# Performance work log

Hardware: AMD Instinct MI355X
Metric: run time of the kernel (lower is better)

Reference implementation:

```python
import jax, jax.numpy as jnp
import numpy as np

B, N, DIM, H, DH, K = 4, 2048, 512, 6, 64, 16
KEEP_PROB = 0.9  # 1 - dropout_rate
LOG2PI = float(np.log(2.0 * np.pi))
LOG_PRIOR = float(np.log(1.0 / K))


def setup_inputs() -> dict:
    key = jax.random.key(0)
    ks = jax.random.split(key, 7)
    inputs_q = jax.random.normal(ks[0], (B, N, DIM), dtype=jnp.float32)
    # decoder-style causal mask, shape [B, 1, q_len, kv_len]
    causal = jnp.tril(jnp.ones((N, N), dtype=jnp.float32))
    mask = jnp.broadcast_to(causal[None, None], (B, 1, N, N))
    # dropout keep mask broadcast across the query dim: [B, H, 1, kv_len]
    keep = jax.random.bernoulli(ks[1], KEEP_PROB, (B, H, 1, N)).astype(jnp.float32)
    w_qkv = jax.random.normal(ks[2], (DIM, 3 * H * DH), dtype=jnp.float32) * 0.02
    w_out = jax.random.normal(ks[3], (H * DH, DIM), dtype=jnp.float32) * 0.02
    mu_lookup = jax.random.normal(ks[4], (K, DIM), dtype=jnp.float32)
    logvar_lookup = jax.random.normal(ks[5], (K, DIM), dtype=jnp.float32) * 0.1
    return {
        "inputs_q": inputs_q,
        "mask": mask,
        "keep": keep,
        "w_qkv": w_qkv,
        "w_out": w_out,
        "mu_lookup": mu_lookup,
        "logvar_lookup": logvar_lookup,
    }


def reference(inputs_q, mask, keep, w_qkv, w_out, mu_lookup, logvar_lookup):
    # --- MultiHeadDotProductAttention (self-attn path) ---
    qkv = (inputs_q @ w_qkv).reshape(B, N, 3, H, DH)  # [B,N,3,H,DH]
    q, k, v = qkv[:, :, 0], qkv[:, :, 1], qkv[:, :, 2]
    # bias: 0 where mask > 0, -1e10 elsewhere (note: no 1/sqrt(d) scaling, as in source)
    bias = jnp.where(mask > 0, 0.0, -1e10)
    attn_weights = jnp.einsum('bqhd,bkhd->bhqk', q, k) + bias  # [B,H,N,N]
    attn_weights = jax.nn.softmax(attn_weights, axis=-1)
    # broadcast dropout: mask shared across the query dim
    attn_weights = attn_weights * keep / KEEP_PROB
    attn_out = jnp.einsum('bhqk,bkhd->bqhd', attn_weights, v)
    attn_out = attn_out.reshape(B, N, H * DH) @ w_out  # [B,N,DIM]

    # --- GMM posterior approx q(y|x) ~= p(y|z) (approx_qy_x, vectorized over k) ---
    z = attn_out.mean(axis=1)  # pooled latent, [B,DIM]
    diff = z[:, None, :] - mu_lookup[None]  # [B,K,DIM]
    llh = -0.5 * jnp.sum(
        diff * diff / jnp.exp(logvar_lookup)[None] + logvar_lookup[None] + LOG2PI,
        axis=-1,
    )  # [B,K]
    logLogit_qy_x = llh + LOG_PRIOR
    qy_x = jax.nn.softmax(logLogit_qy_x, axis=1)  # [B,K]

    # combine mixture mean back in so both branches are live in one output
    return attn_out + (qy_x @ mu_lookup)[:, None, :]
```

## Files before the change

### kernel.cpp

```cpp
#include <hip/hip_runtime.h>
#include <cstdint>
#include <cstddef>

#define NH 6
#define NSEQ 2048
#define DIMD 512
#define BATCH 4
#define HD 384
#define LOG2PI_F 1.8378770664093453f

typedef __attribute__((ext_vector_type(8))) short short8;
typedef __attribute__((ext_vector_type(8))) unsigned short ushort8;
typedef __attribute__((ext_vector_type(4))) unsigned short ushort4v;
typedef __attribute__((ext_vector_type(4))) float floatx4;

__device__ inline unsigned short f2bf(float f){
  unsigned int u = __float_as_uint(f);
  u += 0x7FFFu + ((u>>16)&1u);
  return (unsigned short)(u>>16);
}

#define GLD16(gp, lp) __builtin_amdgcn_global_load_lds( \
  (const __attribute__((address_space(1))) void*)(gp), \
  (__attribute__((address_space(3))) void*)(lp), 16, 0, 0)

__global__ __launch_bounds__(256) void convert_x(
    const float* __restrict__ xq, unsigned short* __restrict__ xbf)
{
  int i = blockIdx.x*256 + threadIdx.x;
  floatx4 v = *(const floatx4*)(xq + (size_t)i*4);
  ushort4v r;
  #pragma unroll
  for(int j=0;j<4;j++) r[j] = f2bf(v[j]);
  *(ushort4v*)(xbf + (size_t)i*4) = r;
}

__global__ __launch_bounds__(256) void wtrans(
    const float* __restrict__ src, unsigned short* __restrict__ dst, int R, int C)
{
  __shared__ __attribute__((aligned(16))) unsigned short Ls[64*72];
  const int t = threadIdx.x;
  const int r = t>>2, c0 = (t&3)*16;
  const int d0 = blockIdx.y*64, n0 = blockIdx.x*64;
  #pragma unroll
  for (int j=0;j<16;j+=4){
    floatx4 v = *(const floatx4*)(src + (size_t)(d0+r)*C + n0 + c0 + j);
    #pragma unroll
    for(int jj=0;jj<4;jj++) Ls[r*72 + c0+j+jj] = f2bf(v[jj]);
  }
  __syncthreads();
  #pragma unroll
  for (int j=0;j<16;j+=8){
    ushort8 o;
    #pragma unroll
    for(int jj=0;jj<8;jj++) o[jj] = Ls[(c0+j+jj)*72 + r];
    *(ushort8*)(dst + (size_t)(n0+r)*R + d0 + c0 + j) = o;
  }
}

__global__ __launch_bounds__(256) void vtrans(
    const unsigned short* __restrict__ Vo, unsigned short* __restrict__ Vt)
{
  __shared__ __attribute__((aligned(16))) unsigned short Ls[64*72];
  const int t = threadIdx.x;
  const int r = t>>2, c0 = (t&3)*16;
  const int n0 = blockIdx.x*64, bh = blockIdx.y;
  #pragma unroll
  for (int j=0;j<16;j+=8)
    *(ushort8*)(Ls + r*72 + c0 + j) = *(const ushort8*)(Vo + ((size_t)bh*NSEQ + n0 + r)*64 + c0 + j);
  __syncthreads();
  #pragma unroll
  for (int j=0;j<16;j+=8){
    ushort8 o;
    #pragma unroll
    for(int jj=0;jj<8;jj++) o[jj] = Ls[(c0+j+jj)*72 + r];
    *(ushort8*)(Vt + ((size_t)bh*64 + r)*NSEQ + n0 + c0 + j) = o;
  }
}

__global__ __launch_bounds__(256) void gemm_qkv(
    const unsigned short* __restrict__ A,
    const unsigned short* __restrict__ Bt,
    const float* __restrict__ keep,
    unsigned short* __restrict__ Qo, unsigned short* __restrict__ Ko, unsigned short* __restrict__ Vo)
{
  __shared__ __attribute__((aligned(16))) unsigned short Cs[128*132];
  unsigned short* As = Cs;
  unsigned short* Bs = Cs + 128*64;
  const int tid = threadIdx.x;
  const int w = tid>>6, lane = tid&63;
  const int wr = w>>1, wc = w&1;
  const int quad = lane>>4, l16 = lane&15;
  const int tM = blockIdx.x*128, tN = blockIdx.y*128;
  const int r8 = lane>>3, c8 = (lane&7)*8;
  floatx4 acc[4][4];
  floatx4 zed = {0.f,0.f,0.f,0.f};
  #pragma unroll
  for (int i=0;i<4;i++)
    #pragma unroll
    for(int j=0;j<4;j++) acc[i][j] = zed;

  for (int k0=0; k0<512; k0+=64){
    #pragma unroll
    for (int i=0;i<4;i++){
      int row = w*32 + i*8;
      GLD16(A  + (size_t)(tM+row+r8)*512 + k0 + c8, As + row*64);
      GLD16(Bt + (size_t)(tN+row+r8)*512 + k0 + c8, Bs + row*64);
    }
    __syncthreads();
    #pragma unroll
    for (int kk=0; kk<64; kk+=32){
      short8 af[4], bf[4];
      #pragma unroll
      for(int mt=0;mt<4;mt++)
        af[mt] = *(const short8*)(As + (wr*64+mt*16+l16)*64 + kk + quad*8);
      #pragma unroll
      for(int nt=0;nt<4;nt++)
        bf[nt] = *(const short8*)(Bs + (wc*64+nt*16+l16)*64 + kk + quad*8);
      #pragma unroll
      for(int mt=0;mt<4;mt++)
        #pragma unroll
        for(int nt=0;nt<4;nt++)
          acc[mt][nt] = __builtin_amdgcn_mfma_f32_16x16x32_bf16(af[mt], bf[nt], acc[mt][nt], 0,0,0);
    }
    __syncthreads();
  }
  #pragma unroll
  for(int mt=0;mt<4;mt++)
    #pragma unroll
    for(int nt=0;nt<4;nt++)
      #pragma unroll
      for(int r=0;r<4;r++)
        Cs[(wr*64+mt*16+quad*4+r)*132 + wc*64+nt*16+l16] = f2bf(acc[mt][nt][r]);
  __syncthreads();
  const int row = tid>>1, colh = (tid&1)*64;
  const int gcol0 = tN + colh;
  const int t = gcol0/384, rem = gcol0 - t*384, h = rem>>6;
  const int grow = tM + row, b = grow>>11, n = grow & 2047;
  unsigned short* dst = (t==0 ? Qo : (t==1 ? Ko : Vo)) + ((size_t)((b*NH+h)*NSEQ+n))*64;
  bool vzero = false;
  if (t==2) vzero = (keep[(size_t)(b*NH+h)*NSEQ+n] < 0.5f);
  ushort8 zz;
  #pragma unroll
  for(int q2=0;q2<8;q2++) zz[q2]=0;
  #pragma unroll
  for(int j=0;j<8;j++){
    ushort8 v = *(const ushort8*)(Cs + row*132 + colh + j*8);
    *(ushort8*)(dst + j*8) = vzero ? zz : v;
  }
}

__global__ __launch_bounds__(64) void attn_kernel(
    const unsigned short* __restrict__ Qg, const unsigned short* __restrict__ Kg,
    const unsigned short* __restrict__ VtG,
    unsigned short* __restrict__ atp)
{
  __shared__ __attribute__((aligned(16))) unsigned short Ps[32*72];
  const int lane = threadIdx.x;
  const int quad = lane>>4, l16 = lane&15;
  const int bid = blockIdx.x;
  const int idx = bid>>3;
  const int bh  = (bid&7) + 8*(idx % 3);
  const int c   = 63 - idx/3;
  const int b = bh/NH, h = bh - b*NH;
  const unsigned short* Qb = Qg  + (size_t)bh*NSEQ*64;
  const unsigned short* Kb = Kg  + (size_t)bh*NSEQ*64;
  const unsigned short* Vb = VtG + (size_t)bh*64*NSEQ;
  const int q0 = c*32;
  const int nkt = (c>>1) + 1;

  short8 qf[2][2];
  #pragma unroll
  for(int mt=0;mt<2;mt++)
    #pragma unroll
    for(int kc=0;kc<2;kc++)
      qf[mt][kc] = *(const short8*)(Qb + (size_t)(q0+mt*16+l16)*64 + kc*32 + quad*8);

  short8 onesf;
  #pragma unroll
  for(int j=0;j<8;j++) onesf[j] = (short)0x3F80;

  floatx4 O[2][4];
  floatx4 accl[2];
  floatx4 zed = {0.f,0.f,0.f,0.f};
  #pragma unroll
  for(int mt=0;mt<2;mt++){
    #pragma unroll
    for(int dt=0;dt<4;dt++) O[mt][dt] = zed;
    accl[mt] = zed;
  }

  short8 kA[4][2], kB2[4][2];
  auto loadK = [&](int kt, short8 (&kf)[4][2]){
    const unsigned short* kp0 = Kb + (size_t)kt*64*64;
    #pragma unroll
    for(int nt=0;nt<4;nt++)
      #pragma unroll
      for(int kc=0;kc<2;kc++)
        kf[nt][kc] = *(const short8*)(kp0 + (size_t)(nt*16+l16)*64 + kc*32 + quad*8);
  };

  auto tile = [&](int kt, short8 (&kf)[4][2]){
    const int kB = kt*64;
    short8 vf[2][4];
    const unsigned short* vp0 = Vb + kB;
    #pragma unroll
    for(int kh=0;kh<2;kh++)
      #pragma unroll
      for(int dt=0;dt<4;dt++)
        vf[kh][dt] = *(const short8*)(vp0 + (size_t)(dt*16+l16)*NSEQ + kh*32 + quad*8);

    floatx4 sacc[2][4];
    floatx4 m12 = {-12.f,-12.f,-12.f,-12.f};
    #pragma unroll
    for(int mt=0;mt<2;mt++)
      #pragma unroll
      for(int nt=0;nt<4;nt++) sacc[mt][nt] = m12;
    #pragma unroll
    for(int mt=0;mt<2;mt++)
      #pragma unroll
      for(int nt=0;nt<4;nt++)
        #pragma unroll
        for(int kc=0;kc<2;kc++)
          sacc[mt][nt] = __builtin_amdgcn_mfma_f32_16x16x32_bf16(qf[mt][kc], kf[nt][kc], sacc[mt][nt], 0,0,0);

    const bool dia = (kt == nkt-1);
    #pragma unroll
    for(int mt=0;mt<2;mt++){
      #pragma unroll
      for(int nt=0;nt<4;nt++){
        int key = kB + nt*16 + l16;
        #pragma unroll
        for(int r=0;r<4;r++){
          float p = __expf(sacc[mt][nt][r]);
          if (dia) p = (key <= q0 + mt*16 + quad*4 + r) ? p : 0.f;
          Ps[(mt*16+quad*4+r)*72 + nt*16 + l16] = f2bf(p);
        }
      }
    }
    #pragma unroll
    for(int kh=0;kh<2;kh++){
      #pragma unroll
      for(int mt=0;mt<2;mt++){
        short8 pf = *(const short8*)(Ps + (mt*16+l16)*72 + kh*32 + quad*8);
        accl[mt] = __builtin_amdgcn_mfma_f32_16x16x32_bf16(pf, onesf, accl[mt], 0,0,0);
        #pragma unroll
        for(int dt=0;dt<4;dt++)
          O[mt][dt] = __builtin_amdgcn_mfma_f32_16x16x32_bf16(pf, vf[kh][dt], O[mt][dt], 0,0,0);
      }
    }
  };

  loadK(0, kA);
  int kt = 0;
  while (true){
    loadK(kt+1 < nkt ? kt+1 : kt, kB2);
    tile(kt, kA);
    kt++; if (kt >= nkt) break;
    loadK(kt+1 < nkt ? kt+1 : kt, kA);
    tile(kt, kB2);
    kt++; if (kt >= nkt) break;
  }

  #pragma unroll
  for(int mt=0;mt<2;mt++)
    #pragma unroll
    for(int r=0;r<4;r++){
      float sc2 = (1.0f/0.9f) / accl[mt][r];
      #pragma unroll
      for(int dt=0;dt<4;dt++)
        Ps[(mt*16+quad*4+r)*72 + dt*16 + l16] = f2bf(O[mt][dt][r]*sc2);
    }
  const int orow = lane>>1, ohalf = (lane&1)*32;
  const int q = q0 + orow;
  unsigned short* dstp = atp + ((size_t)(b*NSEQ+q))*HD + h*64 + ohalf;
  #pragma unroll
  for(int j=0;j<4;j++)
    *(ushort8*)(dstp + j*8) = *(const ushort8*)(Ps + orow*72 + ohalf + j*8);
}

__global__ __launch_bounds__(256) void gemm_proj(
    const unsigned short* __restrict__ A,
    const unsigned short* __restrict__ Bt,
    float* __restrict__ out,
    float* __restrict__ z)
{
  __shared__ __attribute__((aligned(16))) unsigned short As[128*64];
  __shared__ __attribute__((aligned(16))) unsigned short Bs[128*64];
  const int tid = threadIdx.x;
  const int w = tid>>6, lane = tid&63;
  const int wr = w>>1, wc = w&1;
  const int quad = lane>>4, l16 = lane&15;
  const int tM = blockIdx.x*128, tN = blockIdx.y*128;
  const int r8 = lane>>3, c8 = (lane&7)*8;
  floatx4 acc[4][4];
  floatx4 zed = {0.f,0.f,0.f,0.f};
  #pragma unroll
  for (int i=0;i<4;i++)
    #pragma unroll
    for(int j=0;j<4;j++) acc[i][j] = zed;

  for (int k0=0; k0<384; k0+=64){
    #pragma unroll
    for (int i=0;i<4;i++){
      int row = w*32 + i*8;
      GLD16(A  + (size_t)(tM+row+r8)*384 + k0 + c8, As + row*64);
      GLD16(Bt + (size_t)(tN+row+r8)*384 + k0 + c8, Bs + row*64);
    }
    __syncthreads();
    #pragma unroll
    for (int kk=0; kk<64; kk+=32){
      short8 af[4], bf[4];
      #pragma unroll
      for(int mt=0;mt<4;mt++)
        af[mt] = *(const short8*)(As + (wr*64+mt*16+l16)*64 + kk + quad*8);
      #pragma unroll
      for(int nt=0;nt<4;nt++)
        bf[nt] = *(const short8*)(Bs + (wc*64+nt*16+l16)*64 + kk + quad*8);
      #pragma unroll
      for(int mt=0;mt<4;mt++)
        #pragma unroll
        for(int nt=0;nt<4;nt++)
          acc[mt][nt] = __builtin_amdgcn_mfma_f32_16x16x32_bf16(af[mt], bf[nt], acc[mt][nt], 0,0,0);
    }
    __syncthreads();
  }
  #pragma unroll
  for(int mt=0;mt<4;mt++){
    int grow = tM + wr*64 + mt*16 + quad*4;
    #pragma unroll
    for(int nt=0;nt<4;nt++){
      int gcol = tN + wc*64 + nt*16 + l16;
      #pragma unroll
      for(int r=0;r<4;r++)
        out[(size_t)(grow+r)*512 + gcol] = acc[mt][nt][r];
    }
  }
  #pragma unroll
  for(int nt=0;nt<4;nt++){
    float s = 0.f;
    #pragma unroll
    for(int mt=0;mt<4;mt++)
      #pragma unroll
      for(int r=0;r<4;r++) s += acc[mt][nt][r];
    s += __shfl_xor(s, 16, 64);
    s += __shfl_xor(s, 32, 64);
    if (quad == 0){
      int gcol = tN + wc*64 + nt*16 + l16;
      atomicAdd(&z[(tM>>11)*DIMD + gcol], s);
    }
  }
}

__global__ __launch_bounds__(256) void gmm_kernel(
    const float* __restrict__ z, const float* __restrict__ mu,
    const float* __restrict__ lv, float* __restrict__ c)
{
  __shared__ float sh[16];
  __shared__ float qy[16];
  int tid = threadIdx.x;
  int k = tid>>4, li = tid&15;
  int b = blockIdx.x;
  float part = 0.f;
  for(int d=li; d<DIMD; d+=16){
    float zz = z[b*DIMD+d] * (1.0f/2048.0f);
    float m = mu[k*DIMD+d], l = lv[k*DIMD+d];
    float diff = zz - m;
    part += diff*diff*__expf(-l) + l + LOG2PI_F;
  }
  #pragma unroll
  for(int off=8;off>=1;off>>=1) part += __shfl_xor(part, off, 64);
  if (li==0) sh[k] = part;
  __syncthreads();
  if (tid<16){
    float logit = -0.5f*sh[tid];
    float mx = logit;
    #pragma unroll
    for(int off=8;off>=1;off>>=1) mx = fmaxf(mx, __shfl_xor(mx, off, 64));
    float e = __expf(logit-mx);
    float se = e;
    #pragma unroll
    for(int off=8;off>=1;off>>=1) se += __shfl_xor(se, off, 64);
    qy[tid] = e/se;
  }
  __syncthreads();
  for(int d=tid; d<DIMD; d+=256){
    float accv = 0.f;
    #pragma unroll
    for(int kk=0;kk<16;kk++) accv += qy[kk]*mu[kk*DIMD+d];
    c[b*DIMD+d] = accv;
  }
}

__global__ __launch_bounds__(256) void final_add(
    float* __restrict__ out, const float* __restrict__ c)
{
  size_t i = ((size_t)blockIdx.x*256 + threadIdx.x)*4;
  int d = (int)(i & 511);
  int b = (int)(i >> 20);
  floatx4 a = *(const floatx4*)(out + i);
  floatx4 cc = *(const floatx4*)(c + b*DIMD + d);
  *(floatx4*)(out + i) = a + cc;
}

extern "C" void kernel_launch(void* const* d_in, const int* in_sizes, int n_in,
                              void* d_out, int out_size, void* d_ws, size_t ws_size,
                              hipStream_t stream) {
  const float* inputs_q = (const float*)d_in[0];
  const float* keep  = (const float*)d_in[2];
  const float* w_qkv = (const float*)d_in[3];
  const float* w_out = (const float*)d_in[4];
  const float* mu    = (const float*)d_in[5];
  const float* lv    = (const float*)d_in[6];
  float* out = (float*)d_out;
  char* ws = (char*)d_ws;
  size_t off = 0;
  auto alloc = [&](size_t bytes){ void* p = ws + off; off += (bytes + 255) & ~(size_t)255; return p; };
  unsigned short* Qb  = (unsigned short*)alloc((size_t)24*2048*64*2);
  unsigned short* Kb  = (unsigned short*)alloc((size_t)24*2048*64*2);
  unsigned short* Vo  = (unsigned short*)alloc((size_t)24*2048*64*2);
  unsigned short* Vt  = (unsigned short*)alloc((size_t)24*64*2048*2);
  unsigned short* xbf = (unsigned short*)alloc((size_t)8192*512*2);
  unsigned short* wqT = (unsigned short*)alloc((size_t)1152*512*2);
  unsigned short* woT = (unsigned short*)alloc((size_t)512*384*2);
  unsigned short* atp = (unsigned short*)alloc((size_t)8192*384*2);
  float* z  = (float*)alloc((size_t)4*512*4);
  float* c  = (float*)alloc((size_t)4*512*4);

  hipMemsetAsync(z, 0, 4*512*4, stream);
  convert_x<<<4096, 256, 0, stream>>>(inputs_q, xbf);
  wtrans<<<dim3(18,8), 256, 0, stream>>>(w_qkv, wqT, 512, 1152);
  wtrans<<<dim3(8,6),  256, 0, stream>>>(w_out, woT, 384, 512);
  gemm_qkv<<<dim3(64,9), 256, 0, stream>>>(xbf, wqT, keep, Qb, Kb, Vo);
  vtrans<<<dim3(32,24), 256, 0, stream>>>(Vo, Vt);
  attn_kernel<<<1536, 64, 0, stream>>>(Qb, Kb, Vt, atp);
  gemm_proj<<<dim3(64,4), 256, 0, stream>>>(atp, woT, out, z);
  gmm_kernel<<<4, 256, 0, stream>>>(z, mu, lv, c);
  final_add<<<4096, 256, 0, stream>>>(out, c);
}
```

Baseline: 246.3 us.

## Fuse prep kernels, write V transposed from QKV GEMM, pool z in attention

The conversion, weight-transpose and zeroing kernels are merged into one launch. The QKV GEMM now writes V already transposed and dropout-scaled, so the separate vtrans pass and its Vo buffer go away. Attention is cut to 16-query tiles, doubling the number of blocks. Each attention block atomically accumulates its pooled head output into zA, and the GMM kernel computes z by multiplying zA with w_out instead of reading projection outputs. The mixture mean is added in the projection epilogue, which removes the final_add pass over the output. The trade-offs are more atomics, a serial 384-long dot product per column in the GMM kernel, a truncating bf16 conversion of P, and GMM now sitting on the critical path before the projection GEMM.

```diff
diff --git a/kernel.cpp b/kernel.cpp
--- a/kernel.cpp
+++ b/kernel.cpp
@@ -13,6 +13,7 @@
 typedef __attribute__((ext_vector_type(8))) unsigned short ushort8;
 typedef __attribute__((ext_vector_type(4))) unsigned short ushort4v;
 typedef __attribute__((ext_vector_type(4))) float floatx4;
+typedef __attribute__((ext_vector_type(2))) unsigned int uint2v;
 
 __device__ inline unsigned short f2bf(float f){
   unsigned int u = __float_as_uint(f);
@@ -24,57 +25,46 @@
   (const __attribute__((address_space(1))) void*)(gp), \
   (__attribute__((address_space(3))) void*)(lp), 16, 0, 0)
 
-__global__ __launch_bounds__(256) void convert_x(
-    const float* __restrict__ xq, unsigned short* __restrict__ xbf)
-{
-  int i = blockIdx.x*256 + threadIdx.x;
-  floatx4 v = *(const floatx4*)(xq + (size_t)i*4);
-  ushort4v r;
-  #pragma unroll
-  for(int j=0;j<4;j++) r[j] = f2bf(v[j]);
-  *(ushort4v*)(xbf + (size_t)i*4) = r;
-}
-
-__global__ __launch_bounds__(256) void wtrans(
-    const float* __restrict__ src, unsigned short* __restrict__ dst, int R, int C)
+__global__ __launch_bounds__(256) void prep_kernel(
+    const float* __restrict__ xq, const float* __restrict__ wq, const float* __restrict__ wo,
+    unsigned short* __restrict__ xbf, unsigned short* __restrict__ wqT,
+    unsigned short* __restrict__ woT, float* __restrict__ zA)
 {
   __shared__ __attribute__((aligned(16))) unsigned short Ls[64*72];
-  const int t = threadIdx.x;
-  const int r = t>>2, c0 = (t&3)*16;
-  const int d0 = blockIdx.y*64, n0 = blockIdx.x*64;
-  #pragma unroll
-  for (int j=0;j<16;j+=4){
-    floatx4 v = *(const floatx4*)(src + (size_t)(d0+r)*C + n0 + c0 + j);
-    #pragma unroll
-    for(int jj=0;jj<4;jj++) Ls[r*72 + c0+j+jj] = f2bf(v[jj]);
-  }
-  __syncthreads();
-  #pragma unroll
-  for (int j=0;j<16;j+=8){
-    ushort8 o;
-    #pragma unroll
-    for(int jj=0;jj<8;jj++) o[jj] = Ls[(c0+j+jj)*72 + r];
-    *(ushort8*)(dst + (size_t)(n0+r)*R + d0 + c0 + j) = o;
-  }
-}
-
-__global__ __launch_bounds__(256) void vtrans(
-    const unsigned short* __restrict__ Vo, unsigned short* __restrict__ Vt)
-{
-  __shared__ __attribute__((aligned(16))) unsigned short Ls[64*72];
-  const int t = threadIdx.x;
-  const int r = t>>2, c0 = (t&3)*16;
-  const int n0 = blockIdx.x*64, bh = blockIdx.y;
-  #pragma unroll
-  for (int j=0;j<16;j+=8)
-    *(ushort8*)(Ls + r*72 + c0 + j) = *(const ushort8*)(Vo + ((size_t)bh*NSEQ + n0 + r)*64 + c0 + j);
-  __syncthreads();
-  #pragma unroll
-  for (int j=0;j<16;j+=8){
-    ushort8 o;
-    #pragma unroll
-    for(int jj=0;jj<8;jj++) o[jj] = Ls[(c0+j+jj)*72 + r];
-    *(ushort8*)(Vt + ((size_t)bh*64 + r)*NSEQ + n0 + c0 + j) = o;
+  const int bid = blockIdx.x, t = threadIdx.x;
+  if (bid < 4096){
+    int i = bid*256 + t;
+    floatx4 v = *(const floatx4*)(xq + (size_t)i*4);
+    ushort4v r;
+    #pragma unroll
+    for(int j=0;j<4;j++) r[j] = f2bf(v[j]);
+    *(ushort4v*)(xbf + (size_t)i*4) = r;
+  } else if (bid < 4096+144+48){
+    const bool isq = bid < 4096+144;
+    const int j  = isq ? bid-4096 : bid-(4096+144);
+    const int nx = isq ? 18 : 8;
+    const int R  = isq ? 512 : 384, C = isq ? 1152 : 512;
+    const float* src = isq ? wq : wo;
+    unsigned short* dst = isq ? wqT : woT;
+    const int x = j % nx, y = j / nx;
+    const int n0 = x*64, d0 = y*64;
+    const int r = t>>2, c0 = (t&3)*16;
+    #pragma unroll
+    for (int jj=0;jj<16;jj+=4){
+      floatx4 v = *(const floatx4*)(src + (size_t)(d0+r)*C + n0 + c0 + jj);
+      #pragma unroll
+      for(int q=0;q<4;q++) Ls[r*72 + c0+jj+q] = f2bf(v[q]);
+    }
+    __syncthreads();
+    #pragma unroll
+    for (int jj=0;jj<16;jj+=8){
+      ushort8 o;
+      #pragma unroll
+      for(int q=0;q<8;q++) o[q] = Ls[(c0+jj+q)*72 + r];
+      *(ushort8*)(dst + (size_t)(n0+r)*R + d0 + c0 + jj) = o;
+    }
+  } else {
+    for (int i=t; i<BATCH*HD; i+=256) zA[i] = 0.f;
   }
 }
 
@@ -82,16 +72,17 @@
     const unsigned short* __restrict__ A,
     const unsigned short* __restrict__ Bt,
     const float* __restrict__ keep,
-    unsigned short* __restrict__ Qo, unsigned short* __restrict__ Ko, unsigned short* __restrict__ Vo)
+    unsigned short* __restrict__ Qo, unsigned short* __restrict__ Ko, unsigned short* __restrict__ Vt)
 {
-  __shared__ __attribute__((aligned(16))) unsigned short Cs[128*132];
+  __shared__ __attribute__((aligned(16))) unsigned short Cs[128*136];
   unsigned short* As = Cs;
   unsigned short* Bs = Cs + 128*64;
   const int tid = threadIdx.x;
   const int w = tid>>6, lane = tid&63;
   const int wr = w>>1, wc = w&1;
   const int quad = lane>>4, l16 = lane&15;
-  const int tM = blockIdx.x*128, tN = blockIdx.y*128;
+  const int by = blockIdx.y;
+  const int tM = blockIdx.x*128, tN = by*128;
   const int r8 = lane>>3, c8 = (lane&7)*8;
   floatx4 acc[4][4];
   floatx4 zed = {0.f,0.f,0.f,0.f};
@@ -125,70 +116,89 @@
     }
     __syncthreads();
   }
-  #pragma unroll
-  for(int mt=0;mt<4;mt++)
-    #pragma unroll
-    for(int nt=0;nt<4;nt++)
-      #pragma unroll
-      for(int r=0;r<4;r++)
-        Cs[(wr*64+mt*16+quad*4+r)*132 + wc*64+nt*16+l16] = f2bf(acc[mt][nt][r]);
-  __syncthreads();
-  const int row = tid>>1, colh = (tid&1)*64;
-  const int gcol0 = tN + colh;
-  const int t = gcol0/384, rem = gcol0 - t*384, h = rem>>6;
-  const int grow = tM + row, b = grow>>11, n = grow & 2047;
-  unsigned short* dst = (t==0 ? Qo : (t==1 ? Ko : Vo)) + ((size_t)((b*NH+h)*NSEQ+n))*64;
-  bool vzero = false;
-  if (t==2) vzero = (keep[(size_t)(b*NH+h)*NSEQ+n] < 0.5f);
-  ushort8 zz;
-  #pragma unroll
-  for(int q2=0;q2<8;q2++) zz[q2]=0;
-  #pragma unroll
-  for(int j=0;j<8;j++){
-    ushort8 v = *(const ushort8*)(Cs + row*132 + colh + j*8);
-    *(ushort8*)(dst + j*8) = vzero ? zz : v;
+  const int b = tM>>11;
+  if (by < 6){
+    #pragma unroll
+    for(int mt=0;mt<4;mt++)
+      #pragma unroll
+      for(int nt=0;nt<4;nt++)
+        #pragma unroll
+        for(int r=0;r<4;r++)
+          Cs[(wr*64+mt*16+quad*4+r)*132 + wc*64+nt*16+l16] = f2bf(acc[mt][nt][r]);
+    __syncthreads();
+    const int row = tid>>1, colh = (tid&1)*64;
+    const int gcol0 = tN + colh;
+    const int tq = gcol0/384, rem = gcol0 - tq*384, h = rem>>6;
+    const int grow = tM + row, n = grow & 2047;
+    unsigned short* dst = (tq==0 ? Qo : Ko) + ((size_t)((b*NH+h)*NSEQ+n))*64;
+    #pragma unroll
+    for(int j=0;j<8;j++)
+      *(ushort8*)(dst + j*8) = *(const ushort8*)(Cs + row*132 + colh + j*8);
+  } else {
+    const int hbase = (by-6)*2;
+    const float* kp = keep + (size_t)(b*NH + hbase + wc)*NSEQ + (tM & 2047);
+    #pragma unroll
+    for(int mt=0;mt<4;mt++){
+      float kv[4];
+      #pragma unroll
+      for(int r=0;r<4;r++) kv[r] = kp[wr*64+mt*16+quad*4+r];
+      #pragma unroll
+      for(int nt=0;nt<4;nt++){
+        int col = wc*64+nt*16+l16;
+        int row = wr*64+mt*16+quad*4;
+        unsigned int lo = (unsigned int)f2bf(acc[mt][nt][0]*kv[0]) | ((unsigned int)f2bf(acc[mt][nt][1]*kv[1])<<16);
+        unsigned int hi = (unsigned int)f2bf(acc[mt][nt][2]*kv[2]) | ((unsigned int)f2bf(acc[mt][nt][3]*kv[3])<<16);
+        uint2v v2 = {lo, hi};
+        *(uint2v*)(Cs + (size_t)col*136 + row) = v2;
+      }
+    }
+    __syncthreads();
+    const int nu = tid & 15;
+    #pragma unroll
+    for(int vc0=0; vc0<128; vc0+=16){
+      int vtcol = vc0 + (tid>>4);
+      int h2 = hbase + (vtcol>>6), dh = vtcol & 63;
+      unsigned short* dstv = Vt + ((size_t)((b*NH+h2)*64 + dh))*NSEQ + (tM & 2047) + nu*8;
+      *(ushort8*)dstv = *(const ushort8*)(Cs + (size_t)vtcol*136 + nu*8);
+    }
   }
 }
 
 __global__ __launch_bounds__(64) void attn_kernel(
     const unsigned short* __restrict__ Qg, const unsigned short* __restrict__ Kg,
     const unsigned short* __restrict__ VtG,
-    unsigned short* __restrict__ atp)
+    unsigned short* __restrict__ atp,
+    float* __restrict__ zA)
 {
-  __shared__ __attribute__((aligned(16))) unsigned short Ps[32*72];
+  __shared__ __attribute__((aligned(16))) unsigned short Ps[16*72];
   const int lane = threadIdx.x;
   const int quad = lane>>4, l16 = lane&15;
   const int bid = blockIdx.x;
   const int idx = bid>>3;
   const int bh  = (bid&7) + 8*(idx % 3);
-  const int c   = 63 - idx/3;
+  const int c   = 127 - idx/3;
   const int b = bh/NH, h = bh - b*NH;
   const unsigned short* Qb = Qg  + (size_t)bh*NSEQ*64;
   const unsigned short* Kb = Kg  + (size_t)bh*NSEQ*64;
   const unsigned short* Vb = VtG + (size_t)bh*64*NSEQ;
-  const int q0 = c*32;
-  const int nkt = (c>>1) + 1;
-
-  short8 qf[2][2];
-  #pragma unroll
-  for(int mt=0;mt<2;mt++)
-    #pragma unroll
-    for(int kc=0;kc<2;kc++)
-      qf[mt][kc] = *(const short8*)(Qb + (size_t)(q0+mt*16+l16)*64 + kc*32 + quad*8);
+  const int q0 = c*16;
+  const int nkt = (c>>2) + 1;
+
+  short8 qf[2];
+  #pragma unroll
+  for(int kc=0;kc<2;kc++)
+    qf[kc] = *(const short8*)(Qb + (size_t)(q0+l16)*64 + kc*32 + quad*8);
 
   short8 onesf;
   #pragma unroll
   for(int j=0;j<8;j++) onesf[j] = (short)0x3F80;
 
-  floatx4 O[2][4];
-  floatx4 accl[2];
+  floatx4 O[4];
+  floatx4 accl;
   floatx4 zed = {0.f,0.f,0.f,0.f};
   #pragma unroll
-  for(int mt=0;mt<2;mt++){
-    #pragma unroll
-    for(int dt=0;dt<4;dt++) O[mt][dt] = zed;
-    accl[mt] = zed;
-  }
+  for(int dt=0;dt<4;dt++) O[dt] = zed;
+  accl = zed;
 
   short8 kA[4][2], kB2[4][2];
   auto loadK = [&](int kt, short8 (&kf)[4][2]){
@@ -210,44 +220,34 @@
       for(int dt=0;dt<4;dt++)
         vf[kh][dt] = *(const short8*)(vp0 + (size_t)(dt*16+l16)*NSEQ + kh*32 + quad*8);
 
-    floatx4 sacc[2][4];
+    floatx4 sacc[4];
     floatx4 m12 = {-12.f,-12.f,-12.f,-12.f};
     #pragma unroll
-    for(int mt=0;mt<2;mt++)
-      #pragma unroll
-      for(int nt=0;nt<4;nt++) sacc[mt][nt] = m12;
-    #pragma unroll
-    for(int mt=0;mt<2;mt++)
-      #pragma unroll
-      for(int nt=0;nt<4;nt++)
-        #pragma unroll
-        for(int kc=0;kc<2;kc++)
-          sacc[mt][nt] = __builtin_amdgcn_mfma_f32_16x16x32_bf16(qf[mt][kc], kf[nt][kc], sacc[mt][nt], 0,0,0);
+    for(int nt=0;nt<4;nt++) sacc[nt] = m12;
+    #pragma unroll
+    for(int nt=0;nt<4;nt++)
+      #pragma unroll
+      for(int kc=0;kc<2;kc++)
+        sacc[nt] = __builtin_amdgcn_mfma_f32_16x16x32_bf16(qf[kc], kf[nt][kc], sacc[nt], 0,0,0);
 
     const bool dia = (kt == nkt-1);
     #pragma unroll
-    for(int mt=0;mt<2;mt++){
-      #pragma unroll
-      for(int nt=0;nt<4;nt++){
-        int key = kB + nt*16 + l16;
-        #pragma unroll
-        for(int r=0;r<4;r++){
-          float p = __expf(sacc[mt][nt][r]);
-          if (dia) p = (key <= q0 + mt*16 + quad*4 + r) ? p : 0.f;
-          Ps[(mt*16+quad*4+r)*72 + nt*16 + l16] = f2bf(p);
-        }
+    for(int nt=0;nt<4;nt++){
+      int key = kB + nt*16 + l16;
+      #pragma unroll
+      for(int r=0;r<4;r++){
+        float p = __expf(sacc[nt][r]);
+        if (dia) p = (key <= q0 + quad*4 + r) ? p : 0.f;
+        Ps[(quad*4+r)*72 + nt*16 + l16] = (unsigned short)(__float_as_uint(p)>>16);
       }
     }
     #pragma unroll
     for(int kh=0;kh<2;kh++){
-      #pragma unroll
-      for(int mt=0;mt<2;mt++){
-        short8 pf = *(const short8*)(Ps + (mt*16+l16)*72 + kh*32 + quad*8);
-        accl[mt] = __builtin_amdgcn_mfma_f32_16x16x32_bf16(pf, onesf, accl[mt], 0,0,0);
-        #pragma unroll
-        for(int dt=0;dt<4;dt++)
-          O[mt][dt] = __builtin_amdgcn_mfma_f32_16x16x32_bf16(pf, vf[kh][dt], O[mt][dt], 0,0,0);
-      }
+      short8 pf = *(const short8*)(Ps + l16*72 + kh*32 + quad*8);
+      accl = __builtin_amdgcn_mfma_f32_16x16x32_bf16(pf, onesf, accl, 0,0,0);
+      #pragma unroll
+      for(int dt=0;dt<4;dt++)
+        O[dt] = __builtin_amdgcn_mfma_f32_16x16x32_bf16(pf, vf[kh][dt], O[dt], 0,0,0);
     }
   };
 
@@ -262,28 +262,80 @@
     kt++; if (kt >= nkt) break;
   }
 
-  #pragma unroll
-  for(int mt=0;mt<2;mt++)
+  float sc2[4];
+  #pragma unroll
+  for(int r=0;r<4;r++) sc2[r] = (1.0f/0.9f) / accl[r];
+  #pragma unroll
+  for(int dt=0;dt<4;dt++){
+    float s = 0.f;
     #pragma unroll
     for(int r=0;r<4;r++){
-      float sc2 = (1.0f/0.9f) / accl[mt][r];
-      #pragma unroll
-      for(int dt=0;dt<4;dt++)
-        Ps[(mt*16+quad*4+r)*72 + dt*16 + l16] = f2bf(O[mt][dt][r]*sc2);
-    }
-  const int orow = lane>>1, ohalf = (lane&1)*32;
-  const int q = q0 + orow;
-  unsigned short* dstp = atp + ((size_t)(b*NSEQ+q))*HD + h*64 + ohalf;
-  #pragma unroll
-  for(int j=0;j<4;j++)
-    *(ushort8*)(dstp + j*8) = *(const ushort8*)(Ps + orow*72 + ohalf + j*8);
+      float v = O[dt][r]*sc2[r];
+      s += v;
+      Ps[(quad*4+r)*72 + dt*16 + l16] = f2bf(v);
+    }
+    atomicAdd(&zA[b*HD + h*64 + dt*16 + l16], s);
+  }
+  const int orow = lane>>2, oseg = (lane&3)*16;
+  unsigned short* dstp = atp + ((size_t)(b*NSEQ + q0 + orow))*HD + h*64 + oseg;
+  *(ushort8*)(dstp)     = *(const ushort8*)(Ps + orow*72 + oseg);
+  *(ushort8*)(dstp + 8) = *(const ushort8*)(Ps + orow*72 + oseg + 8);
+}
+
+__global__ __launch_bounds__(256) void gmm_kernel(
+    const float* __restrict__ zA, const float* __restrict__ wo,
+    const float* __restrict__ mu, const float* __restrict__ lv, float* __restrict__ c)
+{
+  __shared__ float zAs[HD];
+  __shared__ float zs[DIMD];
+  __shared__ float sh[16];
+  __shared__ float qy[16];
+  const int tid = threadIdx.x;
+  const int b = blockIdx.x;
+  for (int i=tid; i<HD; i+=256) zAs[i] = zA[b*HD + i];
+  __syncthreads();
+  for (int d=tid; d<DIMD; d+=256){
+    float s = 0.f;
+    for (int k=0; k<HD; k++) s += zAs[k]*wo[(size_t)k*DIMD + d];
+    zs[d] = s * (1.0f/2048.0f);
+  }
+  __syncthreads();
+  const int k = tid>>4, li = tid&15;
+  float part = 0.f;
+  for(int d=li; d<DIMD; d+=16){
+    float m = mu[k*DIMD+d], l = lv[k*DIMD+d];
+    float diff = zs[d] - m;
+    part += diff*diff*__expf(-l) + l + LOG2PI_F;
+  }
+  #pragma unroll
+  for(int off=8;off>=1;off>>=1) part += __shfl_xor(part, off, 64);
+  if (li==0) sh[k] = part;
+  __syncthreads();
+  if (tid<16){
+    float logit = -0.5f*sh[tid];
+    float mx = logit;
+    #pragma unroll
+    for(int off=8;off>=1;off>>=1) mx = fmaxf(mx, __shfl_xor(mx, off, 64));
+    float e = __expf(logit-mx);
+    float se = e;
+    #pragma unroll
+    for(int off=8;off>=1;off>>=1) se += __shfl_xor(se, off, 64);
+    qy[tid] = e/se;
+  }
+  __syncthreads();
+  for(int d=tid; d<DIMD; d+=256){
+    float accv = 0.f;
+    #pragma unroll
+    for(int kk=0;kk<16;kk++) accv += qy[kk]*mu[kk*DIMD+d];
+    c[b*DIMD+d] = accv;
+  }
 }
 
 __global__ __launch_bounds__(256) void gemm_proj(
     const unsigned short* __restrict__ A,
     const unsigned short* __restrict__ Bt,
-    float* __restrict__ out,
-    float* __restrict__ z)
+    const float* __restrict__ c,
+    float* __restrict__ out)
 {
   __shared__ __attribute__((aligned(16))) unsigned short As[128*64];
   __shared__ __attribute__((aligned(16))) unsigned short Bs[128*64];
@@ -325,6 +377,10 @@
     }
     __syncthreads();
   }
+  const int b = tM>>11;
+  float cb[4];
+  #pragma unroll
+  for(int nt=0;nt<4;nt++) cb[nt] = c[b*DIMD + tN + wc*64 + nt*16 + l16];
   #pragma unroll
   for(int mt=0;mt<4;mt++){
     int grow = tM + wr*64 + mt*16 + quad*4;
@@ -333,74 +389,9 @@
       int gcol = tN + wc*64 + nt*16 + l16;
       #pragma unroll
       for(int r=0;r<4;r++)
-        out[(size_t)(grow+r)*512 + gcol] = acc[mt][nt][r];
-    }
-  }
-  #pragma unroll
-  for(int nt=0;nt<4;nt++){
-    float s = 0.f;
-    #pragma unroll
-    for(int mt=0;mt<4;mt++)
-      #pragma unroll
-      for(int r=0;r<4;r++) s += acc[mt][nt][r];
-    s += __shfl_xor(s, 16, 64);
-    s += __shfl_xor(s, 32, 64);
-    if (quad == 0){
-      int gcol = tN + wc*64 + nt*16 + l16;
-      atomicAdd(&z[(tM>>11)*DIMD + gcol], s);
-    }
-  }
-}
-
-__global__ __launch_bounds__(256) void gmm_kernel(
-    const float* __restrict__ z, const float* __restrict__ mu,
-    const float* __restrict__ lv, float* __restrict__ c)
-{
-  __shared__ float sh[16];
-  __shared__ float qy[16];
-  int tid = threadIdx.x;
-  int k = tid>>4, li = tid&15;
-  int b = blockIdx.x;
-  float part = 0.f;
-  for(int d=li; d<DIMD; d+=16){
-    float zz = z[b*DIMD+d] * (1.0f/2048.0f);
-    float m = mu[k*DIMD+d], l = lv[k*DIMD+d];
-    float diff = zz - m;
-    part += diff*diff*__expf(-l) + l + LOG2PI_F;
-  }
-  #pragma unroll
-  for(int off=8;off>=1;off>>=1) part += __shfl_xor(part, off, 64);
-  if (li==0) sh[k] = part;
-  __syncthreads();
-  if (tid<16){
-    float logit = -0.5f*sh[tid];
-    float mx = logit;
-    #pragma unroll
-    for(int off=8;off>=1;off>>=1) mx = fmaxf(mx, __shfl_xor(mx, off, 64));
-    float e = __expf(logit-mx);
-    float se = e;
-    #pragma unroll
-    for(int off=8;off>=1;off>>=1) se += __shfl_xor(se, off, 64);
-    qy[tid] = e/se;
-  }
-  __syncthreads();
-  for(int d=tid; d<DIMD; d+=256){
-    float accv = 0.f;
-    #pragma unroll
-    for(int kk=0;kk<16;kk++) accv += qy[kk]*mu[kk*DIMD+d];
-    c[b*DIMD+d] = accv;
-  }
-}
-
-__global__ __launch_bounds__(256) void final_add(
-    float* __restrict__ out, const float* __restrict__ c)
-{
-  size_t i = ((size_t)blockIdx.x*256 + threadIdx.x)*4;
-  int d = (int)(i & 511);
-  int b = (int)(i >> 20);
-  floatx4 a = *(const floatx4*)(out + i);
-  floatx4 cc = *(const floatx4*)(c + b*DIMD + d);
-  *(floatx4*)(out + i) = a + cc;
+        out[(size_t)(grow+r)*512 + gcol] = acc[mt][nt][r] + cb[nt];
+    }
+  }
 }
 
 extern "C" void kernel_launch(void* const* d_in, const int* in_sizes, int n_in,
@@ -418,23 +409,17 @@
   auto alloc = [&](size_t bytes){ void* p = ws + off; off += (bytes + 255) & ~(size_t)255; return p; };
   unsigned short* Qb  = (unsigned short*)alloc((size_t)24*2048*64*2);
   unsigned short* Kb  = (unsigned short*)alloc((size_t)24*2048*64*2);
-  unsigned short* Vo  = (unsigned short*)alloc((size_t)24*2048*64*2);
   unsigned short* Vt  = (unsigned short*)alloc((size_t)24*64*2048*2);
   unsigned short* xbf = (unsigned short*)alloc((size_t)8192*512*2);
   unsigned short* wqT = (unsigned short*)alloc((size_t)1152*512*2);
   unsigned short* woT = (unsigned short*)alloc((size_t)512*384*2);
   unsigned short* atp = (unsigned short*)alloc((size_t)8192*384*2);
-  float* z  = (float*)alloc((size_t)4*512*4);
+  float* zA = (float*)alloc((size_t)4*384*4);
   float* c  = (float*)alloc((size_t)4*512*4);
 
-  hipMemsetAsync(z, 0, 4*512*4, stream);
-  convert_x<<<4096, 256, 0, stream>>>(inputs_q, xbf);
-  wtrans<<<dim3(18,8), 256, 0, stream>>>(w_qkv, wqT, 512, 1152);
-  wtrans<<<dim3(8,6),  256, 0, stream>>>(w_out, woT, 384, 512);
-  gemm_qkv<<<dim3(64,9), 256, 0, stream>>>(xbf, wqT, keep, Qb, Kb, Vo);
-  vtrans<<<dim3(32,24), 256, 0, stream>>>(Vo, Vt);
-  attn_kernel<<<1536, 64, 0, stream>>>(Qb, Kb, Vt, atp);
-  gemm_proj<<<dim3(64,4), 256, 0, stream>>>(atp, woT, out, z);
-  gmm_kernel<<<4, 256, 0, stream>>>(z, mu, lv, c);
-  final_add<<<4096, 256, 0, stream>>>(out, c);
-}
+  prep_kernel<<<4289, 256, 0, stream>>>(inputs_q, w_qkv, w_out, xbf, wqT, woT, zA);
+  gemm_qkv<<<dim3(64,9), 256, 0, stream>>>(xbf, wqT, keep, Qb, Kb, Vt);
+  attn_kernel<<<3072, 64, 0, stream>>>(Qb, Kb, Vt, atp, zA);
+  gmm_kernel<<<4, 256, 0, stream>>>(zA, w_out, mu, lv, c);
+  gemm_proj<<<dim3(64,4), 256, 0, stream>>>(atp, woT, c, out);
+}
```

Measured after the change: 293.3 us. 1.19x slower.
